# Optimization experiments

Hardware: AMD Instinct MI355X
Metric: run time of the kernel (lower is better)

The kernel has to match this reference:

```python
import jax, jax.numpy as jnp
import numpy as np

B, N, C = 8, 4096, 768
NUM_HEADS = 8
HEAD_DIM = C // NUM_HEADS
FOCUSING_FACTOR = 3


def setup_inputs() -> dict:
    key = jax.random.key(0)
    ks = jax.random.split(key, 8)
    x = jax.random.normal(ks[0], (B, N, C), dtype=jnp.float32)
    Wq = jax.random.normal(ks[1], (C, C), dtype=jnp.float32) * 0.02
    Wkv = jax.random.normal(ks[2], (C, C), dtype=jnp.float32) * 0.02
    Wproj = jax.random.normal(ks[3], (C, C), dtype=jnp.float32) * 0.02
    bproj = jnp.zeros((C,), dtype=jnp.float32)
    w_g = jax.random.normal(ks[4], (C, 1), dtype=jnp.float32)
    # scale / positional_encoding are zero-init Parameters; use small random
    # values so the numerics are non-trivial for kernel testing.
    scale_p = jax.random.normal(ks[5], (1, 1, C), dtype=jnp.float32) * 0.02
    pos_enc = jax.random.normal(ks[6], (1, N, C), dtype=jnp.float32) * 0.02
    return {"x": x, "H": 64, "W": 64, "Wq": Wq, "Wkv": Wkv,
            "Wproj": Wproj, "bproj": bproj, "w_g": w_g,
            "scale_p": scale_p, "pos_enc": pos_enc}


def _l2norm(v, axis):
    return jnp.sqrt(jnp.sum(v * v, axis=axis, keepdims=True))


def reference(x, H, W, Wq, Wkv, Wproj, bproj, w_g, scale_p, pos_enc):
    Bx, Nx, Cx = x.shape
    scale_factor = HEAD_DIM ** (-0.5)
    q = jnp.einsum('bnc,dc->bnd', x, Wq)      # (B,N,C)
    k = jnp.einsum('bnc,dc->bnd', x, Wkv)     # kv -> k
    # global aggregation weight
    A = (q @ w_g) * scale_factor              # (B,N,1)
    A = A / jnp.maximum(_l2norm(A, axis=1), 1e-12)  # F.normalize over dim=1
    G = jnp.sum(A * q, axis=1)                # (B,C)
    xg = G[:, None, :] * k                    # (B,N,C)
    k = k + pos_enc
    # focusing feature map
    scale = jax.nn.softplus(scale_p)
    q = (jax.nn.relu(q) + 1e-6) / scale
    k = (jax.nn.relu(k) + 1e-6) / scale
    q_norm = _l2norm(q, axis=-1)
    k_norm = _l2norm(k, axis=-1)
    q = q ** FOCUSING_FACTOR
    k = k ** FOCUSING_FACTOR
    q = q / _l2norm(q, axis=-1) * q_norm
    k = k / _l2norm(k, axis=-1) * k_norm
    # split heads: (B, H, N, d)
    q = q.reshape(Bx, Nx, NUM_HEADS, HEAD_DIM).transpose(0, 2, 1, 3)
    k = k.reshape(Bx, Nx, NUM_HEADS, HEAD_DIM).transpose(0, 2, 1, 3)
    k_mean = k.mean(axis=2)                   # (B,H,d)
    z = 1.0 / (jnp.einsum('bhnd,bhd->bhn', q, k_mean)[..., None] + 1e-6)
    xg = xg.reshape(Bx, Nx, NUM_HEADS, HEAD_DIM).transpose(0, 2, 1, 3)
    xg = xg * z                               # (B,H,N,d)
    out = xg.transpose(0, 2, 1, 3).reshape(Bx, Nx, Cx)
    out = jnp.einsum('bnc,dc->bnd', out, Wproj) + bproj
    return out
```

## Files before the change

kernel.cpp:

```cpp
#include <hip/hip_runtime.h>
#include <hip/hip_bf16.h>
#include <cstdint>
#include <cstddef>


#define GLOAD_LDS16(g, l) \
  __builtin_amdgcn_global_load_lds((const __attribute__((address_space(1))) void*)(g), \
                                   (__attribute__((address_space(3))) void*)(l), 16, 0, 0)

typedef __attribute__((ext_vector_type(8))) short bf16x8;
typedef __attribute__((ext_vector_type(4))) float f32x4;

__device__ __forceinline__ ushort f2bf(float f) {
  union { float f; uint32_t u; } v; v.f = f;
  uint32_t r = v.u + 0x7fffu + ((v.u >> 16) & 1u);
  return (ushort)(r >> 16);
}
__device__ __forceinline__ float bf2f(ushort u) {
  union { uint32_t x; float f; } v; v.x = (uint32_t)u << 16; return v.f;
}

__global__ __launch_bounds__(256) void k_conv(const float* __restrict__ src,
                                              ushort* __restrict__ dst, int n4) {
  int i = blockIdx.x * blockDim.x + threadIdx.x;
  int stride = gridDim.x * blockDim.x;
  for (; i < n4; i += stride) {
    float4 v = ((const float4*)src)[i];
    ushort4 o;
    o.x = f2bf(v.x); o.y = f2bf(v.y); o.z = f2bf(v.z); o.w = f2bf(v.w);
    ((ushort4*)dst)[i] = o;
  }
}

__global__ void k_softplus(const float* __restrict__ p, float* __restrict__ sinv) {
  int i = threadIdx.x + blockIdx.x * 256;
  if (i < 768) {
    float x = p[i];
    float s = (x > 20.f) ? x : log1pf(expf(x));
    sinv[i] = 1.0f / s;
  }
}

template <bool BF16OUT>
__global__ __launch_bounds__(256, 2) void gemm_bt(
    const ushort* __restrict__ A, const ushort* __restrict__ Bt,
    void* __restrict__ Cv, const float* __restrict__ bias, int Ncols, int nbx) {
  constexpr int K = 768, BK = 64;
  __shared__ ushort lA[128 * BK];
  __shared__ ushort lB[128 * BK];
  const int tid  = threadIdx.x;
  const int lane = tid & 63;
  const int w    = tid >> 6;
  const int wr   = w >> 1, wc = w & 1;
  const int cpx  = gridDim.x >> 3;
  const int swz  = (blockIdx.x & 7) * cpx + (blockIdx.x >> 3);
  const int m0 = (swz / nbx) * 128;
  const int n0 = (swz % nbx) * 128;
  const int sr = lane >> 3;
  const int sc = (lane & 7) * 8;

  f32x4 acc[4][4] = {};

  for (int kt = 0; kt < K / BK; ++kt) {
    const int k0 = kt * BK;
    __syncthreads();
#pragma unroll
    for (int i = 0; i < 4; ++i) {
      const int ci = w * 4 + i;
      const int r  = ci * 8 + sr;
      GLOAD_LDS16(A  + (size_t)(m0 + r) * K + (k0 + sc), lA + ci * 512);
      GLOAD_LDS16(Bt + (size_t)(n0 + r) * K + (k0 + sc), lB + ci * 512);
    }
    __syncthreads();
#pragma unroll
    for (int kk = 0; kk < BK / 32; ++kk) {
      bf16x8 af[4], bfr[4];
#pragma unroll
      for (int m = 0; m < 4; ++m)
        af[m] = *(const bf16x8*)&lA[(wr * 64 + m * 16 + (lane & 15)) * BK + kk * 32 + (lane >> 4) * 8];
#pragma unroll
      for (int n = 0; n < 4; ++n)
        bfr[n] = *(const bf16x8*)&lB[(wc * 64 + n * 16 + (lane & 15)) * BK + kk * 32 + (lane >> 4) * 8];
#pragma unroll
      for (int m = 0; m < 4; ++m)
#pragma unroll
        for (int n = 0; n < 4; ++n)
          acc[m][n] = __builtin_amdgcn_mfma_f32_16x16x32_bf16(af[m], bfr[n], acc[m][n], 0, 0, 0);
    }
  }
#pragma unroll
  for (int n = 0; n < 4; ++n) {
    const int col = n0 + wc * 64 + n * 16 + (lane & 15);
    const float bv = (!BF16OUT && bias) ? bias[col] : 0.0f;
#pragma unroll
    for (int m = 0; m < 4; ++m) {
      const int row0 = m0 + wr * 64 + m * 16 + (lane >> 4) * 4;
#pragma unroll
      for (int j = 0; j < 4; ++j) {
        if (BF16OUT)
          ((ushort*)Cv)[(size_t)(row0 + j) * Ncols + col] = f2bf(acc[m][n][j]);
        else
          ((float*)Cv)[(size_t)(row0 + j) * Ncols + col] = acc[m][n][j] + bv;
      }
    }
  }
}

__global__ __launch_bounds__(256) void k_gks(const ushort* __restrict__ qk,
                                             const float* __restrict__ pos,
                                             const float* __restrict__ wg,
                                             const float* __restrict__ sinv,
                                             float* __restrict__ part,
                                             float* __restrict__ partW) {
  __shared__ float pG[4][768];
  __shared__ float pK[4][768];
  __shared__ float lsq[4];
  const int tid = threadIdx.x, lane = tid & 63, w = tid >> 6;
  const int c0 = lane * 12;
  float sv[12], wv[12], ga[12] = {}, ka[12] = {};
#pragma unroll
  for (int v = 0; v < 3; ++v) {
    float4 s = *(const float4*)(sinv + c0 + v * 4);
    float4 g = *(const float4*)(wg + c0 + v * 4);
#pragma unroll
    for (int e = 0; e < 4; ++e) { sv[v * 4 + e] = (&s.x)[e]; wv[v * 4 + e] = (&g.x)[e]; }
  }
  float wsq = 0.f;
  for (int r = 0; r < 8; ++r) {
    const int row = blockIdx.x * 32 + w * 8 + r;
    const ushort* qr = qk + (size_t)row * 1536;
    const float* pr = pos + (size_t)(row & 4095) * 768;
    float q[12], kk[12], u[12];
    float d = 0.f, s1 = 0.f, s2 = 0.f;
#pragma unroll
    for (int v = 0; v < 3; ++v) {
      ushort4 qv = *(const ushort4*)(qr + c0 + v * 4);
      ushort4 kv = *(const ushort4*)(qr + 768 + c0 + v * 4);
      float4 pv = *(const float4*)(pr + c0 + v * 4);
#pragma unroll
      for (int e = 0; e < 4; ++e) {
        const int j = v * 4 + e;
        q[j] = bf2f((&qv.x)[e]);
        kk[j] = bf2f((&kv.x)[e]) + (&pv.x)[e];
      }
    }
#pragma unroll
    for (int j = 0; j < 12; ++j) {
      d += q[j] * wv[j];
      float t = (fmaxf(kk[j], 0.f) + 1e-6f) * sv[j];
      float uu = t * t * t;
      u[j] = uu;
      s1 += t * t; s2 += uu * uu;
    }
#pragma unroll
    for (int m = 32; m; m >>= 1) {
      d += __shfl_xor(d, m); s1 += __shfl_xor(s1, m); s2 += __shfl_xor(s2, m);
    }
    const float ratio = sqrtf(s1 / s2);
    wsq += d * d;
#pragma unroll
    for (int j = 0; j < 12; ++j) { ka[j] += u[j] * ratio; ga[j] += d * q[j]; }
  }
#pragma unroll
  for (int j = 0; j < 12; ++j) { pG[w][c0 + j] = ga[j]; pK[w][c0 + j] = ka[j]; }
  if (lane == 0) lsq[w] = wsq;
  __syncthreads();
  float* outp = part + (size_t)blockIdx.x * 1536;
  for (int i = tid; i < 768; i += 256) {
    outp[i]       = pG[0][i] + pG[1][i] + pG[2][i] + pG[3][i];
    outp[768 + i] = pK[0][i] + pK[1][i] + pK[2][i] + pK[3][i];
  }
  if (tid == 0) partW[blockIdx.x] = lsq[0] + lsq[1] + lsq[2] + lsq[3];
}

__global__ __launch_bounds__(256) void k_rnorm(const float* __restrict__ partW,
                                               float* __restrict__ rnorm) {
  const int tid = threadIdx.x;
  const int b = tid >> 5, j = tid & 31;
  float s = 0.f;
#pragma unroll
  for (int v = 0; v < 4; ++v) s += partW[b * 128 + j * 4 + v];
#pragma unroll
  for (int m = 16; m; m >>= 1) s += __shfl_xor(s, m);
  if (j == 0) {
    const float sf = 0.10206207261596575f;
    rnorm[b] = sf / fmaxf(sf * sqrtf(s), 1e-12f);
  }
}

__global__ __launch_bounds__(256) void k_gred(const float* __restrict__ part,
                                              const float* __restrict__ rnorm,
                                              float* __restrict__ G,
                                              float* __restrict__ ksum) {
  const int i = blockIdx.x * 256 + threadIdx.x;
  const int b = blockIdx.y;
  const float* p = part + (size_t)b * 128 * 1536 + i;
  float s = 0.f;
#pragma unroll 8
  for (int blk = 0; blk < 128; ++blk) s += p[(size_t)blk * 1536];
  if (i < 768) G[b * 768 + i] = s * rnorm[b];
  else         ksum[b * 768 + i - 768] = s;
}

__global__ __launch_bounds__(256) void k_y(const ushort* __restrict__ qk,
                                           const float* __restrict__ G,
                                           const float* __restrict__ ksum,
                                           const float* __restrict__ sinv,
                                           ushort* __restrict__ y) {
  const int tid = threadIdx.x, lane = tid & 63, w = tid >> 6;
  const int row = blockIdx.x * 4 + w;
  const int b = row >> 12;
  const int c0 = lane * 12;
  const ushort* qr = qk + (size_t)row * 1536;
  float kk[12], u[12], ks[12], gg[12];
  float s1 = 0.f, s2 = 0.f;
#pragma unroll
  for (int v = 0; v < 3; ++v) {
    ushort4 qv = *(const ushort4*)(qr + c0 + v * 4);
    ushort4 kv = *(const ushort4*)(qr + 768 + c0 + v * 4);
    float4 sv = *(const float4*)(sinv + c0 + v * 4);
    float4 kv2 = *(const float4*)(ksum + b * 768 + c0 + v * 4);
    float4 gv = *(const float4*)(G + b * 768 + c0 + v * 4);
#pragma unroll
    for (int e = 0; e < 4; ++e) {
      const int j = v * 4 + e;
      kk[j] = bf2f((&kv.x)[e]);
      float t = (fmaxf(bf2f((&qv.x)[e]), 0.f) + 1e-6f) * (&sv.x)[e];
      float uu = t * t * t;
      u[j] = uu; s1 += t * t; s2 += uu * uu;
      ks[j] = (&kv2.x)[e]; gg[j] = (&gv.x)[e];
    }
  }
#pragma unroll
  for (int m = 32; m; m >>= 1) { s1 += __shfl_xor(s1, m); s2 += __shfl_xor(s2, m); }
  const float ratio = sqrtf(s1 / s2);
  float zp = 0.f;
#pragma unroll
  for (int j = 0; j < 12; ++j) zp += u[j] * ks[j];
  zp += __shfl_xor(zp, 1); zp += __shfl_xor(zp, 2); zp += __shfl_xor(zp, 4);
  const float z = 1.0f / (ratio * zp * (1.0f / 4096.0f) + 1e-6f);
  ushort o[12];
#pragma unroll
  for (int j = 0; j < 12; ++j) o[j] = f2bf(gg[j] * kk[j] * z);
  ushort* yp = y + (size_t)row * 768 + c0;
#pragma unroll
  for (int v = 0; v < 3; ++v)
    *(ushort4*)(yp + v * 4) = *(ushort4*)(o + v * 4);
}

extern "C" void kernel_launch(void* const* d_in, const int* in_sizes, int n_in,
                              void* d_out, int out_size, void* d_ws, size_t ws_size,
                              hipStream_t stream) {
  const float* x      = (const float*)d_in[0];
  const float* Wq     = (const float*)d_in[3];
  const float* Wkv    = (const float*)d_in[4];
  const float* Wproj  = (const float*)d_in[5];
  const float* bproj  = (const float*)d_in[6];
  const float* wg     = (const float*)d_in[7];
  const float* scalep = (const float*)d_in[8];
  const float* pos    = (const float*)d_in[9];

  char* ws = (char*)d_ws;
  ushort* qk   = (ushort*)ws;
  ushort* xbf  = (ushort*)(ws + 100663296);
  ushort* ybf  = xbf;
  float*  part = (float*)(ws + 100663296);
  ushort* wqk  = (ushort*)(ws + 150994944);
  ushort* wpj  = (ushort*)(ws + 153354240);
  float*  sinv = (float*)(ws + 154533888);
  float*  partW = (float*)(ws + 154536960);
  float*  accb  = (float*)(ws + 154541056);
  float* Gv     = accb;
  float* ksum   = accb + 6144;
  float* rnorm  = accb + 12288;

  k_conv<<<4096, 256, 0, stream>>>(x, xbf, 25165824 / 4);
  k_conv<<<576, 256, 0, stream>>>(Wq, wqk, 589824 / 4);
  k_conv<<<576, 256, 0, stream>>>(Wkv, wqk + 589824, 589824 / 4);
  k_conv<<<576, 256, 0, stream>>>(Wproj, wpj, 589824 / 4);
  k_softplus<<<3, 256, 0, stream>>>(scalep, sinv);

  gemm_bt<true><<<3072, 256, 0, stream>>>(xbf, wqk, qk, nullptr, 1536, 12);

  k_gks<<<1024, 256, 0, stream>>>(qk, pos, wg, sinv, part, partW);
  k_rnorm<<<1, 256, 0, stream>>>(partW, rnorm);
  k_gred<<<dim3(6, 8), 256, 0, stream>>>(part, rnorm, Gv, ksum);
  k_y<<<8192, 256, 0, stream>>>(qk, Gv, ksum, sinv, ybf);

  gemm_bt<false><<<1536, 256, 0, stream>>>(ybf, wpj, d_out, bproj, 768, 6);
}
```

Before: 398.2 us.

## Use 16-byte coalesced loads in reduction and y kernels; raise GEMM occupancy

The k_gks and k_y kernels change their per-lane column mapping from 12 contiguous elements to an 8-wide chunk plus a 4-wide chunk, so the bf16 q/k reads become 16-byte vector loads that coalesce better across the wave. In k_y the mapping keeps each group of 8 lanes inside one head, so the 8-lane shuffle reduction for z stays correct. Separately, the GEMM launch bound is raised from 2 to 4 blocks per SM, which constrains register usage to allow more resident waves. The tighter register limit risks spills in the 4x4 MFMA accumulator kernel.

```diff
diff --git a/kernel.cpp b/kernel.cpp
--- a/kernel.cpp
+++ b/kernel.cpp
@@ -42,7 +42,7 @@
 }
 
 template <bool BF16OUT>
-__global__ __launch_bounds__(256, 2) void gemm_bt(
+__global__ __launch_bounds__(256, 4) void gemm_bt(
     const ushort* __restrict__ A, const ushort* __restrict__ Bt,
     void* __restrict__ Cv, const float* __restrict__ bias, int Ncols, int nbx) {
   constexpr int K = 768, BK = 64;
@@ -116,41 +116,54 @@
   __shared__ float pK[4][768];
   __shared__ float lsq[4];
   const int tid = threadIdx.x, lane = tid & 63, w = tid >> 6;
-  const int c0 = lane * 12;
-  float sv[12], wv[12], ga[12] = {}, ka[12] = {};
-#pragma unroll
-  for (int v = 0; v < 3; ++v) {
-    float4 s = *(const float4*)(sinv + c0 + v * 4);
-    float4 g = *(const float4*)(wg + c0 + v * 4);
-#pragma unroll
-    for (int e = 0; e < 4; ++e) { sv[v * 4 + e] = (&s.x)[e]; wv[v * 4 + e] = (&g.x)[e]; }
+  const int cA = lane * 8;
+  const int cB = 512 + lane * 4;
+  float svA[8], svB[4], wvA[8], wvB[4];
+  float gaA[8] = {}, gaB[4] = {}, kaA[8] = {}, kaB[4] = {};
+  {
+    float4 s0 = *(const float4*)(sinv + cA);
+    float4 s1v = *(const float4*)(sinv + cA + 4);
+    float4 s2v = *(const float4*)(sinv + cB);
+    float4 g0 = *(const float4*)(wg + cA);
+    float4 g1 = *(const float4*)(wg + cA + 4);
+    float4 g2 = *(const float4*)(wg + cB);
+#pragma unroll
+    for (int e = 0; e < 4; ++e) {
+      svA[e] = (&s0.x)[e]; svA[4 + e] = (&s1v.x)[e]; svB[e] = (&s2v.x)[e];
+      wvA[e] = (&g0.x)[e]; wvA[4 + e] = (&g1.x)[e]; wvB[e] = (&g2.x)[e];
+    }
   }
   float wsq = 0.f;
   for (int r = 0; r < 8; ++r) {
     const int row = blockIdx.x * 32 + w * 8 + r;
     const ushort* qr = qk + (size_t)row * 1536;
     const float* pr = pos + (size_t)(row & 4095) * 768;
-    float q[12], kk[12], u[12];
+    bf16x8 qv8 = *(const bf16x8*)(qr + cA);
+    ushort4 qv4 = *(const ushort4*)(qr + cB);
+    bf16x8 kv8 = *(const bf16x8*)(qr + 768 + cA);
+    ushort4 kv4 = *(const ushort4*)(qr + 768 + cB);
+    float4 p0 = *(const float4*)(pr + cA);
+    float4 p1 = *(const float4*)(pr + cA + 4);
+    float4 p2 = *(const float4*)(pr + cB);
+    float qA[8], qB[4], uA[8], uB[4];
     float d = 0.f, s1 = 0.f, s2 = 0.f;
 #pragma unroll
-    for (int v = 0; v < 3; ++v) {
-      ushort4 qv = *(const ushort4*)(qr + c0 + v * 4);
-      ushort4 kv = *(const ushort4*)(qr + 768 + c0 + v * 4);
-      float4 pv = *(const float4*)(pr + c0 + v * 4);
-#pragma unroll
-      for (int e = 0; e < 4; ++e) {
-        const int j = v * 4 + e;
-        q[j] = bf2f((&qv.x)[e]);
-        kk[j] = bf2f((&kv.x)[e]) + (&pv.x)[e];
-      }
-    }
-#pragma unroll
-    for (int j = 0; j < 12; ++j) {
-      d += q[j] * wv[j];
-      float t = (fmaxf(kk[j], 0.f) + 1e-6f) * sv[j];
+    for (int j = 0; j < 8; ++j) {
+      qA[j] = bf2f((ushort)qv8[j]);
+      float kkv = bf2f((ushort)kv8[j]) + ((j < 4) ? (&p0.x)[j] : (&p1.x)[j - 4]);
+      d += qA[j] * wvA[j];
+      float t = (fmaxf(kkv, 0.f) + 1e-6f) * svA[j];
       float uu = t * t * t;
-      u[j] = uu;
-      s1 += t * t; s2 += uu * uu;
+      uA[j] = uu; s1 += t * t; s2 += uu * uu;
+    }
+#pragma unroll
+    for (int j = 0; j < 4; ++j) {
+      qB[j] = bf2f((&qv4.x)[j]);
+      float kkv = bf2f((&kv4.x)[j]) + (&p2.x)[j];
+      d += qB[j] * wvB[j];
+      float t = (fmaxf(kkv, 0.f) + 1e-6f) * svB[j];
+      float uu = t * t * t;
+      uB[j] = uu; s1 += t * t; s2 += uu * uu;
     }
 #pragma unroll
     for (int m = 32; m; m >>= 1) {
@@ -159,10 +172,14 @@
     const float ratio = sqrtf(s1 / s2);
     wsq += d * d;
 #pragma unroll
-    for (int j = 0; j < 12; ++j) { ka[j] += u[j] * ratio; ga[j] += d * q[j]; }
-  }
-#pragma unroll
-  for (int j = 0; j < 12; ++j) { pG[w][c0 + j] = ga[j]; pK[w][c0 + j] = ka[j]; }
+    for (int j = 0; j < 8; ++j) { kaA[j] += uA[j] * ratio; gaA[j] += d * qA[j]; }
+#pragma unroll
+    for (int j = 0; j < 4; ++j) { kaB[j] += uB[j] * ratio; gaB[j] += d * qB[j]; }
+  }
+#pragma unroll
+  for (int j = 0; j < 8; ++j) { pG[w][cA + j] = gaA[j]; pK[w][cA + j] = kaA[j]; }
+#pragma unroll
+  for (int j = 0; j < 4; ++j) { pG[w][cB + j] = gaB[j]; pK[w][cB + j] = kaB[j]; }
   if (lane == 0) lsq[w] = wsq;
   __syncthreads();
   float* outp = part + (size_t)blockIdx.x * 1536;
@@ -210,25 +227,43 @@
   const int tid = threadIdx.x, lane = tid & 63, w = tid >> 6;
   const int row = blockIdx.x * 4 + w;
   const int b = row >> 12;
-  const int c0 = lane * 12;
+  const int h = lane >> 3, j8 = lane & 7;
+  const int cA = h * 96 + j8 * 8;
+  const int cB = h * 96 + 64 + j8 * 4;
   const ushort* qr = qk + (size_t)row * 1536;
-  float kk[12], u[12], ks[12], gg[12];
+  float kkA[8], kkB[4], uA[8], uB[4], ksA[8], ksB[4], ggA[8], ggB[4];
   float s1 = 0.f, s2 = 0.f;
-#pragma unroll
-  for (int v = 0; v < 3; ++v) {
-    ushort4 qv = *(const ushort4*)(qr + c0 + v * 4);
-    ushort4 kv = *(const ushort4*)(qr + 768 + c0 + v * 4);
-    float4 sv = *(const float4*)(sinv + c0 + v * 4);
-    float4 kv2 = *(const float4*)(ksum + b * 768 + c0 + v * 4);
-    float4 gv = *(const float4*)(G + b * 768 + c0 + v * 4);
-#pragma unroll
-    for (int e = 0; e < 4; ++e) {
-      const int j = v * 4 + e;
-      kk[j] = bf2f((&kv.x)[e]);
-      float t = (fmaxf(bf2f((&qv.x)[e]), 0.f) + 1e-6f) * (&sv.x)[e];
+  {
+    bf16x8 qv8 = *(const bf16x8*)(qr + cA);
+    ushort4 qv4 = *(const ushort4*)(qr + cB);
+    bf16x8 kv8 = *(const bf16x8*)(qr + 768 + cA);
+    ushort4 kv4 = *(const ushort4*)(qr + 768 + cB);
+    float4 s0 = *(const float4*)(sinv + cA);
+    float4 s1v = *(const float4*)(sinv + cA + 4);
+    float4 s2v = *(const float4*)(sinv + cB);
+    float4 k0 = *(const float4*)(ksum + b * 768 + cA);
+    float4 k1 = *(const float4*)(ksum + b * 768 + cA + 4);
+    float4 k2 = *(const float4*)(ksum + b * 768 + cB);
+    float4 g0 = *(const float4*)(G + b * 768 + cA);
+    float4 g1 = *(const float4*)(G + b * 768 + cA + 4);
+    float4 g2 = *(const float4*)(G + b * 768 + cB);
+#pragma unroll
+    for (int j = 0; j < 8; ++j) {
+      kkA[j] = bf2f((ushort)kv8[j]);
+      float sv = (j < 4) ? (&s0.x)[j] : (&s1v.x)[j - 4];
+      float t = (fmaxf(bf2f((ushort)qv8[j]), 0.f) + 1e-6f) * sv;
       float uu = t * t * t;
-      u[j] = uu; s1 += t * t; s2 += uu * uu;
-      ks[j] = (&kv2.x)[e]; gg[j] = (&gv.x)[e];
+      uA[j] = uu; s1 += t * t; s2 += uu * uu;
+      ksA[j] = (j < 4) ? (&k0.x)[j] : (&k1.x)[j - 4];
+      ggA[j] = (j < 4) ? (&g0.x)[j] : (&g1.x)[j - 4];
+    }
+#pragma unroll
+    for (int j = 0; j < 4; ++j) {
+      kkB[j] = bf2f((&kv4.x)[j]);
+      float t = (fmaxf(bf2f((&qv4.x)[j]), 0.f) + 1e-6f) * (&s2v.x)[j];
+      float uu = t * t * t;
+      uB[j] = uu; s1 += t * t; s2 += uu * uu;
+      ksB[j] = (&k2.x)[j]; ggB[j] = (&g2.x)[j];
     }
   }
 #pragma unroll
@@ -236,16 +271,20 @@
   const float ratio = sqrtf(s1 / s2);
   float zp = 0.f;
 #pragma unroll
-  for (int j = 0; j < 12; ++j) zp += u[j] * ks[j];
+  for (int j = 0; j < 8; ++j) zp += uA[j] * ksA[j];
+#pragma unroll
+  for (int j = 0; j < 4; ++j) zp += uB[j] * ksB[j];
   zp += __shfl_xor(zp, 1); zp += __shfl_xor(zp, 2); zp += __shfl_xor(zp, 4);
   const float z = 1.0f / (ratio * zp * (1.0f / 4096.0f) + 1e-6f);
-  ushort o[12];
-#pragma unroll
-  for (int j = 0; j < 12; ++j) o[j] = f2bf(gg[j] * kk[j] * z);
-  ushort* yp = y + (size_t)row * 768 + c0;
-#pragma unroll
-  for (int v = 0; v < 3; ++v)
-    *(ushort4*)(yp + v * 4) = *(ushort4*)(o + v * 4);
+  ushort oA[8], oB[4];
+#pragma unroll
+  for (int j = 0; j < 8; ++j) oA[j] = f2bf(ggA[j] * kkA[j] * z);
+#pragma unroll
+  for (int j = 0; j < 4; ++j) oB[j] = f2bf(ggB[j] * kkB[j] * z);
+  ushort* yp = y + (size_t)row * 768;
+  *(ushort4*)(yp + cA)     = *(ushort4*)(oA);
+  *(ushort4*)(yp + cA + 4) = *(ushort4*)(oA + 4);
+  *(ushort4*)(yp + cB)     = *(ushort4*)(oB);
 }
 
 extern "C" void kernel_launch(void* const* d_in, const int* in_sizes, int n_in,
```

Measured after the change: 395.1 us. No clear change (-0.8%).
